# Optimization experiments

Measured on AMD Instinct MI355X. Metric: run time of the kernel, lower is better.

## Reference

```python
import jax, jax.numpy as jnp
import numpy as np


def _conv1x1(x_flat, W, b):
    # x_flat: [B, Cin, N], W: [Cout, Cin], b: [Cout]
    return jnp.einsum('oc,bcn->bon', W, x_flat) + b[None, :, None]


def setup_inputs() -> dict:
    key = jax.random.key(0)
    ks = jax.random.split(key, 7)
    B, C, H, W = 8, 64, 64, 64
    Ch = C // 2
    s_in = 1.0 / np.sqrt(C)
    x = jax.random.normal(ks[0], (B, C, H, W), dtype=jnp.float32)
    Wb = jax.random.uniform(ks[1], (Ch, C), jnp.float32, -s_in, s_in)
    bb = jax.random.uniform(ks[2], (Ch,), jnp.float32, -s_in, s_in)
    Wc = jax.random.uniform(ks[3], (Ch, C), jnp.float32, -s_in, s_in)
    bc = jax.random.uniform(ks[4], (Ch,), jnp.float32, -s_in, s_in)
    Wd = jax.random.uniform(ks[5], (C, C), jnp.float32, -s_in, s_in)
    bd = jax.random.uniform(ks[6], (C,), jnp.float32, -s_in, s_in)
    return {'x': x, 'Wb': Wb, 'bb': bb, 'Wc': Wc, 'bc': bc, 'Wd': Wd, 'bd': bd}


def reference(x, Wb, bb, Wc, bc, Wd, bd):
    B, C, H, Wd_ = x.shape
    N = H * Wd_
    x_flat = x.reshape(B, C, N)
    feat_b = _conv1x1(x_flat, Wb, bb)            # [B, C/2, N]
    feat_c = _conv1x1(x_flat, Wc, bc)            # [B, C/2, N]
    # scores[b,n,m] = sum_c feat_b[b,c,n] * feat_c[b,c,m]
    scores = jnp.einsum('bcn,bcm->bnm', feat_b, feat_c)
    attn = jax.nn.softmax(scores, axis=-1)       # [B, N, N]
    feat_d = _conv1x1(x_flat, Wd, bd)            # [B, C, N]
    # feat_e[b,c,m] = sum_n feat_d[b,c,n] * attn[b,m,n]  (bmm with attn^T)
    feat_e = jnp.einsum('bcn,bmn->bcm', feat_d, attn)
    return feat_e.reshape(B, C, H, Wd_) + x
```

## Files before the change

kernel.cpp:

```cpp
#include <hip/hip_runtime.h>

#define N_TOK 4096
#define L2E 1.44269504088896340736f

typedef short bf16x8 __attribute__((ext_vector_type(8)));
typedef float f32x4 __attribute__((ext_vector_type(4)));
typedef float f32x16 __attribute__((ext_vector_type(16)));
typedef unsigned int u32x4 __attribute__((ext_vector_type(4)));
typedef unsigned short u16x4 __attribute__((ext_vector_type(4)));

static __device__ __forceinline__ unsigned short f2bf(float f) {
    unsigned int u = __builtin_bit_cast(unsigned int, f);
    u += 0x7FFFu + ((u >> 16) & 1u);
    return (unsigned short)(u >> 16);
}

__global__ __launch_bounds__(256) void proj_kernel(
    const float* __restrict__ x,
    const float* __restrict__ Wb, const float* __restrict__ bb,
    const float* __restrict__ Wc, const float* __restrict__ bc,
    const float* __restrict__ Wd, const float* __restrict__ bd,
    unsigned short* __restrict__ Qg, unsigned short* __restrict__ Kg,
    unsigned short* __restrict__ VgT)
{
    const int b   = blockIdx.y;
    const int n0  = blockIdx.x * 64;
    const int tid = threadIdx.x;

    __shared__ unsigned short Wl[128 * 72];
    __shared__ unsigned short xT[64 * 72];
    __shared__ float bl[128];

    #pragma unroll
    for (int i = 0; i < 32; ++i) {
        int e = i * 256 + tid;
        int row = e >> 6, c = e & 63;
        float v;
        if (row < 32)      v = Wb[row * 64 + c];
        else if (row < 64) v = Wc[(row - 32) * 64 + c];
        else               v = Wd[(row - 64) * 64 + c];
        Wl[row * 72 + c] = f2bf(v);
    }
    if (tid < 128) {
        float v;
        if (tid < 32)      v = bb[tid];
        else if (tid < 64) v = bc[tid - 32];
        else               v = bd[tid - 64];
        bl[tid] = v;
    }
    #pragma unroll
    for (int i = 0; i < 16; ++i) {
        int e = i * 256 + tid;
        int c = e >> 6, nn = e & 63;
        xT[nn * 72 + c] = f2bf(x[((b * 64 + c) << 12) + n0 + nn]);
    }
    __syncthreads();

    const int w = tid >> 6, l = tid & 63;
    const int lrow = l & 15, lk = (l >> 4) * 8;

    const f32x4 vzero = {0.f, 0.f, 0.f, 0.f};
    f32x4 acc[2][4];
    #pragma unroll
    for (int rt = 0; rt < 2; ++rt)
        #pragma unroll
        for (int ct = 0; ct < 4; ++ct)
            acc[rt][ct] = vzero;

    #pragma unroll
    for (int kb = 0; kb < 2; ++kb) {
        bf16x8 af[2];
        #pragma unroll
        for (int rt = 0; rt < 2; ++rt)
            af[rt] = *(const bf16x8*)&Wl[(w * 32 + rt * 16 + lrow) * 72 + kb * 32 + lk];
        #pragma unroll
        for (int ct = 0; ct < 4; ++ct) {
            bf16x8 bfr = *(const bf16x8*)&xT[(ct * 16 + lrow) * 72 + kb * 32 + lk];
            #pragma unroll
            for (int rt = 0; rt < 2; ++rt)
                acc[rt][ct] = __builtin_amdgcn_mfma_f32_16x16x32_bf16(af[rt], bfr, acc[rt][ct], 0, 0, 0);
        }
    }

    #pragma unroll
    for (int rt = 0; rt < 2; ++rt) {
        const int row0 = w * 32 + rt * 16 + ((l >> 4) << 2);
        #pragma unroll
        for (int ct = 0; ct < 4; ++ct) {
            const int n = n0 + ct * 16 + lrow;
            if (row0 < 64) {
                u16x4 pk;
                #pragma unroll
                for (int r = 0; r < 4; ++r) {
                    float v = acc[rt][ct][r] + bl[row0 + r];
                    if (row0 < 32) v *= L2E;
                    pk[r] = f2bf(v);
                }
                unsigned short* dst = (row0 < 32)
                    ? Qg + (size_t)(b * N_TOK + n) * 32 + row0
                    : Kg + (size_t)(b * N_TOK + n) * 32 + (row0 - 32);
                *(u16x4*)dst = pk;
            } else {
                #pragma unroll
                for (int r = 0; r < 4; ++r)
                    VgT[((size_t)(b * 64 + row0 - 64 + r) << 12) + n] =
                        f2bf(acc[rt][ct][r] + bl[row0 + r]);
            }
        }
    }
}

template <int NHALF>
__global__ __launch_bounds__(256) void attn_kernel(
    const unsigned short* __restrict__ Qg,
    const unsigned short* __restrict__ Kg,
    const unsigned short* __restrict__ VgT,
    const float* __restrict__ x,
    float* __restrict__ outp,
    float* __restrict__ Opart,
    float* __restrict__ Ppart)
{
    const int nwg = 256 * NHALF;
    int i = blockIdx.x;
    int wg = (i & 7) * (nwg >> 3) + (i >> 3);
    const int b    = wg / (32 * NHALF);
    const int rem  = wg % (32 * NHALF);
    const int half = (NHALF >= 2) ? (rem >> 5) : 0;
    const int qblk = (NHALF >= 2) ? (rem & 31) : rem;
    const int q0   = qblk * 128;
    const int jbase = half * (N_TOK / NHALF);
    const int NT    = (N_TOK / NHALF) / 64;

    const int tid = threadIdx.x;
    const int w  = tid >> 6, l = tid & 63;
    const int lc = l & 31, hi = l >> 5;

    __shared__ unsigned short Kl[2][64 * 36];
    __shared__ unsigned short Vt[2][64 * 68];
    __shared__ float den[4][32];

    bf16x8 qf[2];
    #pragma unroll
    for (int kb = 0; kb < 2; ++kb)
        qf[kb] = *(const bf16x8*)&Qg[(size_t)(b * N_TOK + q0 + w * 32 + lc) * 32 + kb * 16 + hi * 8];

    const int kj = tid >> 2, kseg = (tid & 3) * 8;
    const int vc = tid >> 2, vj   = (tid & 3) * 16;
    const size_t kbase = (size_t)(b * N_TOK + jbase + kj) * 32 + kseg;
    const size_t vbase = ((size_t)(b * 64 + vc) << 12) + jbase + vj;

    u32x4 kreg, vreg0, vreg1;

    kreg  = *(const u32x4*)&Kg[kbase];
    vreg0 = *(const u32x4*)&VgT[vbase];
    vreg1 = *(const u32x4*)&VgT[vbase + 8];
    *(u32x4*)&Kl[0][kj * 36 + kseg]   = kreg;
    *(u32x4*)&Vt[0][vc * 68 + vj]     = vreg0;
    *(u32x4*)&Vt[0][vc * 68 + vj + 8] = vreg1;
    if (NT > 1) {
        kreg  = *(const u32x4*)&Kg[kbase + 64 * 32];
        vreg0 = *(const u32x4*)&VgT[vbase + 64];
        vreg1 = *(const u32x4*)&VgT[vbase + 64 + 8];
    }
    __syncthreads();

    const f32x16 z16 = {0.f,0.f,0.f,0.f,0.f,0.f,0.f,0.f,0.f,0.f,0.f,0.f,0.f,0.f,0.f,0.f};
    f32x16 o[2] = {z16, z16};
    float psum = 0.f;

    for (int t = 0; t < NT; ++t) {
        const int cur = t & 1;

        f32x16 s[2];
        __builtin_amdgcn_s_setprio(1);
        #pragma unroll
        for (int jt = 0; jt < 2; ++jt) {
            bf16x8 kf0 = *(const bf16x8*)&Kl[cur][(jt * 32 + lc) * 36 + hi * 8];
            bf16x8 kf1 = *(const bf16x8*)&Kl[cur][(jt * 32 + lc) * 36 + 16 + hi * 8];
            s[jt] = __builtin_amdgcn_mfma_f32_32x32x16_bf16(kf0, qf[0], z16, 0, 0, 0);
            s[jt] = __builtin_amdgcn_mfma_f32_32x32x16_bf16(kf1, qf[1], s[jt], 0, 0, 0);
        }
        __builtin_amdgcn_s_setprio(0);

        unsigned paw[4][4];
        #pragma unroll
        for (int jt = 0; jt < 2; ++jt) {
            float pp[16];
            #pragma unroll
            for (int r = 0; r < 16; ++r) {
                float pv = __builtin_amdgcn_exp2f(s[jt][r]);
                psum += pv;
                pp[r] = pv;
            }
            #pragma unroll
            for (int kb2 = 0; kb2 < 2; ++kb2) {
                const int e = kb2 * 8;
                unsigned A, B, C, D;
                asm("v_cvt_pk_bf16_f32 %0, %1, %2" : "=v"(A) : "v"(pp[e + 0]), "v"(pp[e + 1]));
                asm("v_cvt_pk_bf16_f32 %0, %1, %2" : "=v"(B) : "v"(pp[e + 2]), "v"(pp[e + 3]));
                asm("v_cvt_pk_bf16_f32 %0, %1, %2" : "=v"(C) : "v"(pp[e + 4]), "v"(pp[e + 5]));
                asm("v_cvt_pk_bf16_f32 %0, %1, %2" : "=v"(D) : "v"(pp[e + 6]), "v"(pp[e + 7]));
                asm("v_permlane32_swap_b32 %0, %1" : "+v"(A), "+v"(C));
                asm("v_permlane32_swap_b32 %0, %1" : "+v"(B), "+v"(D));
                paw[jt * 2 + kb2][0] = A; paw[jt * 2 + kb2][1] = B;
                paw[jt * 2 + kb2][2] = C; paw[jt * 2 + kb2][3] = D;
            }
        }

        if (t + 1 < NT) {
            const int alt = cur ^ 1;
            *(u32x4*)&Kl[alt][kj * 36 + kseg]   = kreg;
            *(u32x4*)&Vt[alt][vc * 68 + vj]     = vreg0;
            *(u32x4*)&Vt[alt][vc * 68 + vj + 8] = vreg1;
            if (t + 2 < NT) {
                const int j2 = (t + 2) * 64;
                kreg  = *(const u32x4*)&Kg[kbase + (size_t)j2 * 32];
                vreg0 = *(const u32x4*)&VgT[vbase + j2];
                vreg1 = *(const u32x4*)&VgT[vbase + j2 + 8];
            }
        }

        __builtin_amdgcn_s_setprio(1);
        #pragma unroll
        for (int kb = 0; kb < 4; ++kb) {
            u32x4 pw = {paw[kb][0], paw[kb][1], paw[kb][2], paw[kb][3]};
            bf16x8 pa = __builtin_bit_cast(bf16x8, pw);
            #pragma unroll
            for (int cb = 0; cb < 2; ++cb) {
                bf16x8 vf = *(const bf16x8*)&Vt[cur][(cb * 32 + lc) * 68 + kb * 16 + hi * 8];
                o[cb] = __builtin_amdgcn_mfma_f32_32x32x16_bf16(pa, vf, o[cb], 0, 0, 0);
            }
        }
        __builtin_amdgcn_s_setprio(0);
        __syncthreads();
    }

    float tot = psum + __shfl_xor(psum, 32, 64);

    if (NHALF == 1) {
        if (hi == 0) den[w][lc] = __builtin_amdgcn_rcpf(tot);
        __syncthreads();
        #pragma unroll
        for (int cb = 0; cb < 2; ++cb) {
            const int c = cb * 32 + lc;
            #pragma unroll
            for (int g2 = 0; g2 < 4; ++g2) {
                const int qb = q0 + w * 32 + g2 * 8 + hi * 4;
                f32x4 rinv = *(const f32x4*)&den[w][g2 * 8 + hi * 4];
                const size_t idx = (size_t)(b * 64 + c) * N_TOK + qb;
                f32x4 xv = *(const f32x4*)&x[idx];
                f32x4 ov;
                #pragma unroll
                for (int r = 0; r < 4; ++r)
                    ov[r] = o[cb][g2 * 4 + r] * rinv[r] + xv[r];
                *(f32x4*)&outp[idx] = ov;
            }
        }
    } else {
        #pragma unroll
        for (int cb = 0; cb < 2; ++cb) {
            const size_t cidx = (size_t)((half * 8 + b) * 64 + cb * 32 + lc) * N_TOK;
            #pragma unroll
            for (int g2 = 0; g2 < 4; ++g2) {
                const int qb = q0 + w * 32 + g2 * 8 + hi * 4;
                f32x4 ov = {o[cb][g2 * 4 + 0], o[cb][g2 * 4 + 1],
                            o[cb][g2 * 4 + 2], o[cb][g2 * 4 + 3]};
                *(f32x4*)&Opart[cidx + qb] = ov;
            }
        }
        if (hi == 0)
            Ppart[(size_t)(half * 8 + b) * N_TOK + q0 + w * 32 + lc] = tot;
    }
}

template <int NHALF>
__global__ __launch_bounds__(256) void combine_kernel(
    const float* __restrict__ Opart, const float* __restrict__ Ppart,
    const float* __restrict__ x, float* __restrict__ outp)
{
    const int i = blockIdx.x * 256 + threadIdx.x;
    const int q  = (i & 1023) << 2;
    const int bc = i >> 10;
    const int b  = bc >> 6;
    const size_t obase = ((size_t)bc << 12) + q;

    f32x4 osum = {0.f, 0.f, 0.f, 0.f};
    f32x4 psum = {0.f, 0.f, 0.f, 0.f};
    #pragma unroll
    for (int h = 0; h < NHALF; ++h) {
        f32x4 oh = *(const f32x4*)&Opart[((size_t)h << 21) + obase];
        f32x4 ph = *(const f32x4*)&Ppart[((size_t)(h * 8 + b) << 12) + q];
        #pragma unroll
        for (int r = 0; r < 4; ++r) { osum[r] += oh[r]; psum[r] += ph[r]; }
    }
    f32x4 xv = *(const f32x4*)&x[obase];
    f32x4 ov;
    #pragma unroll
    for (int r = 0; r < 4; ++r)
        ov[r] = osum[r] * __builtin_amdgcn_rcpf(psum[r]) + xv[r];
    *(f32x4*)&outp[obase] = ov;
}

extern "C" void kernel_launch(void* const* d_in, const int* in_sizes, int n_in,
                              void* d_out, int out_size, void* d_ws, size_t ws_size,
                              hipStream_t stream) {
    const float* x  = (const float*)d_in[0];
    const float* Wb = (const float*)d_in[1];
    const float* bb = (const float*)d_in[2];
    const float* Wc = (const float*)d_in[3];
    const float* bc = (const float*)d_in[4];
    const float* Wd = (const float*)d_in[5];
    const float* bd = (const float*)d_in[6];
    float* out = (float*)d_out;

    unsigned short* Qg  = (unsigned short*)d_ws;
    unsigned short* Kg  = Qg + (size_t)8 * N_TOK * 32;
    unsigned short* VgT = Kg + (size_t)8 * N_TOK * 32;
    float* Opart = (float*)((char*)d_ws + (size_t)8 * 1024 * 1024);

    proj_kernel<<<dim3(64, 8), 256, 0, stream>>>(x, Wb, bb, Wc, bc, Wd, bd, Qg, Kg, VgT);

    if (ws_size >= (size_t)41 * 1024 * 1024) {
        float* Ppart = (float*)((char*)d_ws + (size_t)40 * 1024 * 1024);
        attn_kernel<4><<<1024, 256, 0, stream>>>(Qg, Kg, VgT, x, out, Opart, Ppart);
        combine_kernel<4><<<2048, 256, 0, stream>>>(Opart, Ppart, x, out);
    } else if (ws_size >= (size_t)25 * 1024 * 1024) {
        float* Ppart = (float*)((char*)d_ws + (size_t)24 * 1024 * 1024);
        attn_kernel<2><<<512, 256, 0, stream>>>(Qg, Kg, VgT, x, out, Opart, Ppart);
        combine_kernel<2><<<2048, 256, 0, stream>>>(Opart, Ppart, x, out);
    } else {
        attn_kernel<1><<<256, 256, 0, stream>>>(Qg, Kg, VgT, x, out, nullptr, nullptr);
    }
}
```

Baseline: 62.12 us.

## Use single-wave attention blocks reading K/V directly, store bf16 partials

```diff
diff --git a/kernel.cpp b/kernel.cpp
--- a/kernel.cpp
+++ b/kernel.cpp
@@ -13,6 +13,9 @@
     unsigned int u = __builtin_bit_cast(unsigned int, f);
     u += 0x7FFFu + ((u >> 16) & 1u);
     return (unsigned short)(u >> 16);
+}
+static __device__ __forceinline__ float bf2f(unsigned short v) {
+    return __builtin_bit_cast(float, ((unsigned)v) << 16);
 }
 
 __global__ __launch_bounds__(256) void proj_kernel(
@@ -111,85 +114,68 @@
 }
 
 template <int NHALF>
-__global__ __launch_bounds__(256) void attn_kernel(
+__global__ __launch_bounds__(64, 4) void attn_kernel(
     const unsigned short* __restrict__ Qg,
     const unsigned short* __restrict__ Kg,
     const unsigned short* __restrict__ VgT,
     const float* __restrict__ x,
     float* __restrict__ outp,
-    float* __restrict__ Opart,
+    unsigned short* __restrict__ Opart,
     float* __restrict__ Ppart)
 {
-    const int nwg = 256 * NHALF;
-    int i = blockIdx.x;
-    int wg = (i & 7) * (nwg >> 3) + (i >> 3);
-    const int b    = wg / (32 * NHALF);
-    const int rem  = wg % (32 * NHALF);
-    const int half = (NHALF >= 2) ? (rem >> 5) : 0;
-    const int qblk = (NHALF >= 2) ? (rem & 31) : rem;
-    const int q0   = qblk * 128;
+    const int nwg = 1024 * NHALF;
+    const int i0 = blockIdx.x;
+    const int wg = (i0 & 7) * (nwg >> 3) + (i0 >> 3);
+    const int bpb  = 128 * NHALF;
+    const int b    = wg / bpb;
+    const int rem  = wg % bpb;
+    const int half = (NHALF == 1) ? 0 : (rem >> 7);
+    const int qblk = rem & 127;
+    const int q0   = qblk * 32;
     const int jbase = half * (N_TOK / NHALF);
     const int NT    = (N_TOK / NHALF) / 64;
 
     const int tid = threadIdx.x;
-    const int w  = tid >> 6, l = tid & 63;
-    const int lc = l & 31, hi = l >> 5;
-
-    __shared__ unsigned short Kl[2][64 * 36];
-    __shared__ unsigned short Vt[2][64 * 68];
-    __shared__ float den[4][32];
-
-    bf16x8 qf[2];
-    #pragma unroll
-    for (int kb = 0; kb < 2; ++kb)
-        qf[kb] = *(const bf16x8*)&Qg[(size_t)(b * N_TOK + q0 + w * 32 + lc) * 32 + kb * 16 + hi * 8];
-
-    const int kj = tid >> 2, kseg = (tid & 3) * 8;
-    const int vc = tid >> 2, vj   = (tid & 3) * 16;
-    const size_t kbase = (size_t)(b * N_TOK + jbase + kj) * 32 + kseg;
-    const size_t vbase = ((size_t)(b * 64 + vc) << 12) + jbase + vj;
-
-    u32x4 kreg, vreg0, vreg1;
-
-    kreg  = *(const u32x4*)&Kg[kbase];
-    vreg0 = *(const u32x4*)&VgT[vbase];
-    vreg1 = *(const u32x4*)&VgT[vbase + 8];
-    *(u32x4*)&Kl[0][kj * 36 + kseg]   = kreg;
-    *(u32x4*)&Vt[0][vc * 68 + vj]     = vreg0;
-    *(u32x4*)&Vt[0][vc * 68 + vj + 8] = vreg1;
-    if (NT > 1) {
-        kreg  = *(const u32x4*)&Kg[kbase + 64 * 32];
-        vreg0 = *(const u32x4*)&VgT[vbase + 64];
-        vreg1 = *(const u32x4*)&VgT[vbase + 64 + 8];
-    }
-    __syncthreads();
+    const int lc = tid & 31, hi = tid >> 5;
+
+    __shared__ float den[32];
+
+    const unsigned short* qp = Qg + (size_t)(b * N_TOK + q0 + lc) * 32 + hi * 8;
+    const bf16x8 qf0 = *(const bf16x8*)qp;
+    const bf16x8 qf1 = *(const bf16x8*)(qp + 16);
+
+    const unsigned short* Kb = Kg + (size_t)(b * N_TOK + jbase) * 32;
+    const unsigned short* Vb = VgT + ((size_t)(b * 64) << 12) + jbase;
 
     const f32x16 z16 = {0.f,0.f,0.f,0.f,0.f,0.f,0.f,0.f,0.f,0.f,0.f,0.f,0.f,0.f,0.f,0.f};
-    f32x16 o[2] = {z16, z16};
-    float psum = 0.f;
+    f32x16 o0 = z16, o1 = z16;
+    float ps0 = 0.f, ps1 = 0.f;
 
     for (int t = 0; t < NT; ++t) {
-        const int cur = t & 1;
-
-        f32x16 s[2];
+        const int j0 = t * 64;
+
+        const unsigned short* kp = Kb + (size_t)(j0 + lc) * 32 + hi * 8;
+        bf16x8 k00 = *(const bf16x8*)(kp);
+        bf16x8 k01 = *(const bf16x8*)(kp + 16);
+        bf16x8 k10 = *(const bf16x8*)(kp + 32 * 32);
+        bf16x8 k11 = *(const bf16x8*)(kp + 32 * 32 + 16);
+
         __builtin_amdgcn_s_setprio(1);
+        f32x16 s0 = __builtin_amdgcn_mfma_f32_32x32x16_bf16(k00, qf0, z16, 0, 0, 0);
+        s0 = __builtin_amdgcn_mfma_f32_32x32x16_bf16(k01, qf1, s0, 0, 0, 0);
+        f32x16 s1 = __builtin_amdgcn_mfma_f32_32x32x16_bf16(k10, qf0, z16, 0, 0, 0);
+        s1 = __builtin_amdgcn_mfma_f32_32x32x16_bf16(k11, qf1, s1, 0, 0, 0);
+        __builtin_amdgcn_s_setprio(0);
+
+        u32x4 pa[4];
         #pragma unroll
         for (int jt = 0; jt < 2; ++jt) {
-            bf16x8 kf0 = *(const bf16x8*)&Kl[cur][(jt * 32 + lc) * 36 + hi * 8];
-            bf16x8 kf1 = *(const bf16x8*)&Kl[cur][(jt * 32 + lc) * 36 + 16 + hi * 8];
-            s[jt] = __builtin_amdgcn_mfma_f32_32x32x16_bf16(kf0, qf[0], z16, 0, 0, 0);
-            s[jt] = __builtin_amdgcn_mfma_f32_32x32x16_bf16(kf1, qf[1], s[jt], 0, 0, 0);
-        }
-        __builtin_amdgcn_s_setprio(0);
-
-        unsigned paw[4][4];
-        #pragma unroll
-        for (int jt = 0; jt < 2; ++jt) {
+            const f32x16& sv = jt ? s1 : s0;
             float pp[16];
             #pragma unroll
             for (int r = 0; r < 16; ++r) {
-                float pv = __builtin_amdgcn_exp2f(s[jt][r]);
-                psum += pv;
+                float pv = __builtin_amdgcn_exp2f(sv[r]);
+                if (r & 1) ps1 += pv; else ps0 += pv;
                 pp[r] = pv;
             }
             #pragma unroll
@@ -202,80 +188,70 @@
                 asm("v_cvt_pk_bf16_f32 %0, %1, %2" : "=v"(D) : "v"(pp[e + 6]), "v"(pp[e + 7]));
                 asm("v_permlane32_swap_b32 %0, %1" : "+v"(A), "+v"(C));
                 asm("v_permlane32_swap_b32 %0, %1" : "+v"(B), "+v"(D));
-                paw[jt * 2 + kb2][0] = A; paw[jt * 2 + kb2][1] = B;
-                paw[jt * 2 + kb2][2] = C; paw[jt * 2 + kb2][3] = D;
-            }
-        }
-
-        if (t + 1 < NT) {
-            const int alt = cur ^ 1;
-            *(u32x4*)&Kl[alt][kj * 36 + kseg]   = kreg;
-            *(u32x4*)&Vt[alt][vc * 68 + vj]     = vreg0;
-            *(u32x4*)&Vt[alt][vc * 68 + vj + 8] = vreg1;
-            if (t + 2 < NT) {
-                const int j2 = (t + 2) * 64;
-                kreg  = *(const u32x4*)&Kg[kbase + (size_t)j2 * 32];
-                vreg0 = *(const u32x4*)&VgT[vbase + j2];
-                vreg1 = *(const u32x4*)&VgT[vbase + j2 + 8];
-            }
-        }
-
+                pa[jt * 2 + kb2][0] = A; pa[jt * 2 + kb2][1] = B;
+                pa[jt * 2 + kb2][2] = C; pa[jt * 2 + kb2][3] = D;
+            }
+        }
+
+        const unsigned short* vp = Vb + ((size_t)lc << 12) + j0 + hi * 8;
         __builtin_amdgcn_s_setprio(1);
         #pragma unroll
         for (int kb = 0; kb < 4; ++kb) {
-            u32x4 pw = {paw[kb][0], paw[kb][1], paw[kb][2], paw[kb][3]};
-            bf16x8 pa = __builtin_bit_cast(bf16x8, pw);
-            #pragma unroll
-            for (int cb = 0; cb < 2; ++cb) {
-                bf16x8 vf = *(const bf16x8*)&Vt[cur][(cb * 32 + lc) * 68 + kb * 16 + hi * 8];
-                o[cb] = __builtin_amdgcn_mfma_f32_32x32x16_bf16(pa, vf, o[cb], 0, 0, 0);
-            }
+            bf16x8 pf = __builtin_bit_cast(bf16x8, pa[kb]);
+            bf16x8 vf0 = *(const bf16x8*)(vp + kb * 16);
+            bf16x8 vf1 = *(const bf16x8*)(vp + ((size_t)32 << 12) + kb * 16);
+            o0 = __builtin_amdgcn_mfma_f32_32x32x16_bf16(pf, vf0, o0, 0, 0, 0);
+            o1 = __builtin_amdgcn_mfma_f32_32x32x16_bf16(pf, vf1, o1, 0, 0, 0);
         }
         __builtin_amdgcn_s_setprio(0);
+    }
+
+    float ps = ps0 + ps1;
+    float tot = ps + __shfl_xor(ps, 32, 64);
+
+    if (NHALF == 1) {
+        if (hi == 0) den[lc] = __builtin_amdgcn_rcpf(tot);
         __syncthreads();
-    }
-
-    float tot = psum + __shfl_xor(psum, 32, 64);
-
-    if (NHALF == 1) {
-        if (hi == 0) den[w][lc] = __builtin_amdgcn_rcpf(tot);
-        __syncthreads();
         #pragma unroll
         for (int cb = 0; cb < 2; ++cb) {
+            const f32x16& ov16 = cb ? o1 : o0;
             const int c = cb * 32 + lc;
             #pragma unroll
             for (int g2 = 0; g2 < 4; ++g2) {
-                const int qb = q0 + w * 32 + g2 * 8 + hi * 4;
-                f32x4 rinv = *(const f32x4*)&den[w][g2 * 8 + hi * 4];
+                const int qb = q0 + g2 * 8 + hi * 4;
+                f32x4 rinv = *(const f32x4*)&den[g2 * 8 + hi * 4];
                 const size_t idx = (size_t)(b * 64 + c) * N_TOK + qb;
                 f32x4 xv = *(const f32x4*)&x[idx];
                 f32x4 ov;
                 #pragma unroll
                 for (int r = 0; r < 4; ++r)
-                    ov[r] = o[cb][g2 * 4 + r] * rinv[r] + xv[r];
+                    ov[r] = ov16[g2 * 4 + r] * rinv[r] + xv[r];
                 *(f32x4*)&outp[idx] = ov;
             }
         }
     } else {
         #pragma unroll
         for (int cb = 0; cb < 2; ++cb) {
-            const size_t cidx = (size_t)((half * 8 + b) * 64 + cb * 32 + lc) * N_TOK;
+            const f32x16& ov16 = cb ? o1 : o0;
+            unsigned short* obase =
+                Opart + ((size_t)((half * 8 + b) * 64 + cb * 32 + lc) << 12);
             #pragma unroll
             for (int g2 = 0; g2 < 4; ++g2) {
-                const int qb = q0 + w * 32 + g2 * 8 + hi * 4;
-                f32x4 ov = {o[cb][g2 * 4 + 0], o[cb][g2 * 4 + 1],
-                            o[cb][g2 * 4 + 2], o[cb][g2 * 4 + 3]};
-                *(f32x4*)&Opart[cidx + qb] = ov;
+                const int qb = q0 + g2 * 8 + hi * 4;
+                u16x4 pk;
+                #pragma unroll
+                for (int r = 0; r < 4; ++r) pk[r] = f2bf(ov16[g2 * 4 + r]);
+                *(u16x4*)(obase + qb) = pk;
             }
         }
         if (hi == 0)
-            Ppart[(size_t)(half * 8 + b) * N_TOK + q0 + w * 32 + lc] = tot;
+            Ppart[((size_t)(half * 8 + b) << 12) + q0 + lc] = tot;
     }
 }
 
 template <int NHALF>
 __global__ __launch_bounds__(256) void combine_kernel(
-    const float* __restrict__ Opart, const float* __restrict__ Ppart,
+    const unsigned short* __restrict__ Opart, const float* __restrict__ Ppart,
     const float* __restrict__ x, float* __restrict__ outp)
 {
     const int i = blockIdx.x * 256 + threadIdx.x;
@@ -288,10 +264,10 @@
     f32x4 psum = {0.f, 0.f, 0.f, 0.f};
     #pragma unroll
     for (int h = 0; h < NHALF; ++h) {
-        f32x4 oh = *(const f32x4*)&Opart[((size_t)h << 21) + obase];
-        f32x4 ph = *(const f32x4*)&Ppart[((size_t)(h * 8 + b) << 12) + q];
-        #pragma unroll
-        for (int r = 0; r < 4; ++r) { osum[r] += oh[r]; psum[r] += ph[r]; }
+        u16x4 oh = *(const u16x4*)&Opart[(((size_t)(h * 512 + bc)) << 12) + q];
+        f32x4 ph = *(const f32x4*)&Ppart[(((size_t)(h * 8 + b)) << 12) + q];
+        #pragma unroll
+        for (int r = 0; r < 4; ++r) { osum[r] += bf2f(oh[r]); psum[r] += ph[r]; }
     }
     f32x4 xv = *(const f32x4*)&x[obase];
     f32x4 ov;
@@ -316,19 +292,15 @@
     unsigned short* Qg  = (unsigned short*)d_ws;
     unsigned short* Kg  = Qg + (size_t)8 * N_TOK * 32;
     unsigned short* VgT = Kg + (size_t)8 * N_TOK * 32;
-    float* Opart = (float*)((char*)d_ws + (size_t)8 * 1024 * 1024);
+    unsigned short* Opart = (unsigned short*)((char*)d_ws + (size_t)8 * 1024 * 1024);
+    float* Ppart = (float*)((char*)d_ws + (size_t)24 * 1024 * 1024);
 
     proj_kernel<<<dim3(64, 8), 256, 0, stream>>>(x, Wb, bb, Wc, bc, Wd, bd, Qg, Kg, VgT);
 
-    if (ws_size >= (size_t)41 * 1024 * 1024) {
-        float* Ppart = (float*)((char*)d_ws + (size_t)40 * 1024 * 1024);
-        attn_kernel<4><<<1024, 256, 0, stream>>>(Qg, Kg, VgT, x, out, Opart, Ppart);
+    if (ws_size >= (size_t)25 * 1024 * 1024) {
+        attn_kernel<4><<<4096, 64, 0, stream>>>(Qg, Kg, VgT, x, out, Opart, Ppart);
         combine_kernel<4><<<2048, 256, 0, stream>>>(Opart, Ppart, x, out);
-    } else if (ws_size >= (size_t)25 * 1024 * 1024) {
-        float* Ppart = (float*)((char*)d_ws + (size_t)24 * 1024 * 1024);
-        attn_kernel<2><<<512, 256, 0, stream>>>(Qg, Kg, VgT, x, out, Opart, Ppart);
-        combine_kernel<2><<<2048, 256, 0, stream>>>(Opart, Ppart, x, out);
     } else {
-        attn_kernel<1><<<256, 256, 0, stream>>>(Qg, Kg, VgT, x, out, nullptr, nullptr);
-    }
-}
+        attn_kernel<1><<<1024, 64, 0, stream>>>(Qg, Kg, VgT, x, out, nullptr, nullptr);
+    }
+}
```

Result: slower. 98.90 us (+59.2%).

## Software-pipeline QK MFMA across tiles, interleave exp with PV, store partials in bf16

Applied to the files above, without the earlier changes.

```diff
diff --git a/kernel.cpp b/kernel.cpp
--- a/kernel.cpp
+++ b/kernel.cpp
@@ -13,6 +13,9 @@
     unsigned int u = __builtin_bit_cast(unsigned int, f);
     u += 0x7FFFu + ((u >> 16) & 1u);
     return (unsigned short)(u >> 16);
+}
+static __device__ __forceinline__ float bf2f(unsigned short v) {
+    return __builtin_bit_cast(float, ((unsigned)v) << 16);
 }
 
 __global__ __launch_bounds__(256) void proj_kernel(
@@ -117,7 +120,7 @@
     const unsigned short* __restrict__ VgT,
     const float* __restrict__ x,
     float* __restrict__ outp,
-    float* __restrict__ Opart,
+    unsigned short* __restrict__ Opart,
     float* __restrict__ Ppart)
 {
     const int nwg = 256 * NHALF;
@@ -139,10 +142,9 @@
     __shared__ unsigned short Vt[2][64 * 68];
     __shared__ float den[4][32];
 
-    bf16x8 qf[2];
-    #pragma unroll
-    for (int kb = 0; kb < 2; ++kb)
-        qf[kb] = *(const bf16x8*)&Qg[(size_t)(b * N_TOK + q0 + w * 32 + lc) * 32 + kb * 16 + hi * 8];
+    const unsigned short* qp = Qg + (size_t)(b * N_TOK + q0 + w * 32 + lc) * 32 + hi * 8;
+    const bf16x8 qf0 = *(const bf16x8*)qp;
+    const bf16x8 qf1 = *(const bf16x8*)(qp + 16);
 
     const int kj = tid >> 2, kseg = (tid & 3) * 8;
     const int vc = tid >> 2, vj   = (tid & 3) * 16;
@@ -165,83 +167,91 @@
     __syncthreads();
 
     const f32x16 z16 = {0.f,0.f,0.f,0.f,0.f,0.f,0.f,0.f,0.f,0.f,0.f,0.f,0.f,0.f,0.f,0.f};
-    f32x16 o[2] = {z16, z16};
-    float psum = 0.f;
+    f32x16 o0 = z16, o1 = z16;
+    f32x16 s0, s1;
+    float ps0 = 0.f, ps1 = 0.f;
+
+    {
+        __builtin_amdgcn_s_setprio(1);
+        bf16x8 a00 = *(const bf16x8*)&Kl[0][(lc) * 36 + hi * 8];
+        bf16x8 a01 = *(const bf16x8*)&Kl[0][(lc) * 36 + 16 + hi * 8];
+        bf16x8 a10 = *(const bf16x8*)&Kl[0][(32 + lc) * 36 + hi * 8];
+        bf16x8 a11 = *(const bf16x8*)&Kl[0][(32 + lc) * 36 + 16 + hi * 8];
+        s0 = __builtin_amdgcn_mfma_f32_32x32x16_bf16(a00, qf0, z16, 0, 0, 0);
+        s0 = __builtin_amdgcn_mfma_f32_32x32x16_bf16(a01, qf1, s0, 0, 0, 0);
+        s1 = __builtin_amdgcn_mfma_f32_32x32x16_bf16(a10, qf0, z16, 0, 0, 0);
+        s1 = __builtin_amdgcn_mfma_f32_32x32x16_bf16(a11, qf1, s1, 0, 0, 0);
+        __builtin_amdgcn_s_setprio(0);
+    }
 
     for (int t = 0; t < NT; ++t) {
         const int cur = t & 1;
 
-        f32x16 s[2];
-        __builtin_amdgcn_s_setprio(1);
-        #pragma unroll
-        for (int jt = 0; jt < 2; ++jt) {
-            bf16x8 kf0 = *(const bf16x8*)&Kl[cur][(jt * 32 + lc) * 36 + hi * 8];
-            bf16x8 kf1 = *(const bf16x8*)&Kl[cur][(jt * 32 + lc) * 36 + 16 + hi * 8];
-            s[jt] = __builtin_amdgcn_mfma_f32_32x32x16_bf16(kf0, qf[0], z16, 0, 0, 0);
-            s[jt] = __builtin_amdgcn_mfma_f32_32x32x16_bf16(kf1, qf[1], s[jt], 0, 0, 0);
-        }
-        __builtin_amdgcn_s_setprio(0);
-
-        unsigned paw[4][4];
-        #pragma unroll
-        for (int jt = 0; jt < 2; ++jt) {
-            float pp[16];
+        if (t + 1 < NT) {
+            *(u32x4*)&Kl[cur ^ 1][kj * 36 + kseg]   = kreg;
+            *(u32x4*)&Vt[cur ^ 1][vc * 68 + vj]     = vreg0;
+            *(u32x4*)&Vt[cur ^ 1][vc * 68 + vj + 8] = vreg1;
+        }
+        if (t + 2 < NT) {
+            const int j2 = (t + 2) * 64;
+            kreg  = *(const u32x4*)&Kg[kbase + (size_t)j2 * 32];
+            vreg0 = *(const u32x4*)&VgT[vbase + j2];
+            vreg1 = *(const u32x4*)&VgT[vbase + j2 + 8];
+        }
+
+        #pragma unroll
+        for (int kb = 0; kb < 4; ++kb) {
+            const f32x16& sv = (kb >> 1) ? s1 : s0;
+            const int e = (kb & 1) * 8;
+            float p[8];
             #pragma unroll
-            for (int r = 0; r < 16; ++r) {
-                float pv = __builtin_amdgcn_exp2f(s[jt][r]);
-                psum += pv;
-                pp[r] = pv;
+            for (int r = 0; r < 8; ++r) {
+                p[r] = __builtin_amdgcn_exp2f(sv[e + r]);
+                if (r & 1) ps1 += p[r]; else ps0 += p[r];
             }
-            #pragma unroll
-            for (int kb2 = 0; kb2 < 2; ++kb2) {
-                const int e = kb2 * 8;
-                unsigned A, B, C, D;
-                asm("v_cvt_pk_bf16_f32 %0, %1, %2" : "=v"(A) : "v"(pp[e + 0]), "v"(pp[e + 1]));
-                asm("v_cvt_pk_bf16_f32 %0, %1, %2" : "=v"(B) : "v"(pp[e + 2]), "v"(pp[e + 3]));
-                asm("v_cvt_pk_bf16_f32 %0, %1, %2" : "=v"(C) : "v"(pp[e + 4]), "v"(pp[e + 5]));
-                asm("v_cvt_pk_bf16_f32 %0, %1, %2" : "=v"(D) : "v"(pp[e + 6]), "v"(pp[e + 7]));
-                asm("v_permlane32_swap_b32 %0, %1" : "+v"(A), "+v"(C));
-                asm("v_permlane32_swap_b32 %0, %1" : "+v"(B), "+v"(D));
-                paw[jt * 2 + kb2][0] = A; paw[jt * 2 + kb2][1] = B;
-                paw[jt * 2 + kb2][2] = C; paw[jt * 2 + kb2][3] = D;
-            }
-        }
+            unsigned A, B, C, D;
+            asm("v_cvt_pk_bf16_f32 %0, %1, %2" : "=v"(A) : "v"(p[0]), "v"(p[1]));
+            asm("v_cvt_pk_bf16_f32 %0, %1, %2" : "=v"(B) : "v"(p[2]), "v"(p[3]));
+            asm("v_cvt_pk_bf16_f32 %0, %1, %2" : "=v"(C) : "v"(p[4]), "v"(p[5]));
+            asm("v_cvt_pk_bf16_f32 %0, %1, %2" : "=v"(D) : "v"(p[6]), "v"(p[7]));
+            asm("v_permlane32_swap_b32 %0, %1" : "+v"(A), "+v"(C));
+            asm("v_permlane32_swap_b32 %0, %1" : "+v"(B), "+v"(D));
+            u32x4 pw = {A, B, C, D};
+            bf16x8 pf = __builtin_bit_cast(bf16x8, pw);
+            bf16x8 vf0 = *(const bf16x8*)&Vt[cur][(lc) * 68 + kb * 16 + hi * 8];
+            bf16x8 vf1 = *(const bf16x8*)&Vt[cur][(32 + lc) * 68 + kb * 16 + hi * 8];
+            __builtin_amdgcn_s_setprio(1);
+            o0 = __builtin_amdgcn_mfma_f32_32x32x16_bf16(pf, vf0, o0, 0, 0, 0);
+            o1 = __builtin_amdgcn_mfma_f32_32x32x16_bf16(pf, vf1, o1, 0, 0, 0);
+            __builtin_amdgcn_s_setprio(0);
+        }
+
+        __syncthreads();
 
         if (t + 1 < NT) {
-            const int alt = cur ^ 1;
-            *(u32x4*)&Kl[alt][kj * 36 + kseg]   = kreg;
-            *(u32x4*)&Vt[alt][vc * 68 + vj]     = vreg0;
-            *(u32x4*)&Vt[alt][vc * 68 + vj + 8] = vreg1;
-            if (t + 2 < NT) {
-                const int j2 = (t + 2) * 64;
-                kreg  = *(const u32x4*)&Kg[kbase + (size_t)j2 * 32];
-                vreg0 = *(const u32x4*)&VgT[vbase + j2];
-                vreg1 = *(const u32x4*)&VgT[vbase + j2 + 8];
-            }
-        }
-
-        __builtin_amdgcn_s_setprio(1);
-        #pragma unroll
-        for (int kb = 0; kb < 4; ++kb) {
-            u32x4 pw = {paw[kb][0], paw[kb][1], paw[kb][2], paw[kb][3]};
-            bf16x8 pa = __builtin_bit_cast(bf16x8, pw);
-            #pragma unroll
-            for (int cb = 0; cb < 2; ++cb) {
-                bf16x8 vf = *(const bf16x8*)&Vt[cur][(cb * 32 + lc) * 68 + kb * 16 + hi * 8];
-                o[cb] = __builtin_amdgcn_mfma_f32_32x32x16_bf16(pa, vf, o[cb], 0, 0, 0);
-            }
-        }
-        __builtin_amdgcn_s_setprio(0);
-        __syncthreads();
-    }
-
-    float tot = psum + __shfl_xor(psum, 32, 64);
+            const int nxt = cur ^ 1;
+            __builtin_amdgcn_s_setprio(1);
+            bf16x8 a00 = *(const bf16x8*)&Kl[nxt][(lc) * 36 + hi * 8];
+            bf16x8 a01 = *(const bf16x8*)&Kl[nxt][(lc) * 36 + 16 + hi * 8];
+            bf16x8 a10 = *(const bf16x8*)&Kl[nxt][(32 + lc) * 36 + hi * 8];
+            bf16x8 a11 = *(const bf16x8*)&Kl[nxt][(32 + lc) * 36 + 16 + hi * 8];
+            s0 = __builtin_amdgcn_mfma_f32_32x32x16_bf16(a00, qf0, z16, 0, 0, 0);
+            s0 = __builtin_amdgcn_mfma_f32_32x32x16_bf16(a01, qf1, s0, 0, 0, 0);
+            s1 = __builtin_amdgcn_mfma_f32_32x32x16_bf16(a10, qf0, z16, 0, 0, 0);
+            s1 = __builtin_amdgcn_mfma_f32_32x32x16_bf16(a11, qf1, s1, 0, 0, 0);
+            __builtin_amdgcn_s_setprio(0);
+        }
+    }
+
+    float ps = ps0 + ps1;
+    float tot = ps + __shfl_xor(ps, 32, 64);
 
     if (NHALF == 1) {
         if (hi == 0) den[w][lc] = __builtin_amdgcn_rcpf(tot);
         __syncthreads();
         #pragma unroll
         for (int cb = 0; cb < 2; ++cb) {
+            const f32x16& ov16 = cb ? o1 : o0;
             const int c = cb * 32 + lc;
             #pragma unroll
             for (int g2 = 0; g2 < 4; ++g2) {
@@ -252,30 +262,33 @@
                 f32x4 ov;
                 #pragma unroll
                 for (int r = 0; r < 4; ++r)
-                    ov[r] = o[cb][g2 * 4 + r] * rinv[r] + xv[r];
+                    ov[r] = ov16[g2 * 4 + r] * rinv[r] + xv[r];
                 *(f32x4*)&outp[idx] = ov;
             }
         }
     } else {
         #pragma unroll
         for (int cb = 0; cb < 2; ++cb) {
-            const size_t cidx = (size_t)((half * 8 + b) * 64 + cb * 32 + lc) * N_TOK;
+            const f32x16& ov16 = cb ? o1 : o0;
+            unsigned short* obase =
+                Opart + ((size_t)((half * 8 + b) * 64 + cb * 32 + lc) << 12);
             #pragma unroll
             for (int g2 = 0; g2 < 4; ++g2) {
                 const int qb = q0 + w * 32 + g2 * 8 + hi * 4;
-                f32x4 ov = {o[cb][g2 * 4 + 0], o[cb][g2 * 4 + 1],
-                            o[cb][g2 * 4 + 2], o[cb][g2 * 4 + 3]};
-                *(f32x4*)&Opart[cidx + qb] = ov;
+                u16x4 pk;
+                #pragma unroll
+                for (int r = 0; r < 4; ++r) pk[r] = f2bf(ov16[g2 * 4 + r]);
+                *(u16x4*)(obase + qb) = pk;
             }
         }
         if (hi == 0)
-            Ppart[(size_t)(half * 8 + b) * N_TOK + q0 + w * 32 + lc] = tot;
+            Ppart[((size_t)(half * 8 + b) << 12) + q0 + w * 32 + lc] = tot;
     }
 }
 
 template <int NHALF>
 __global__ __launch_bounds__(256) void combine_kernel(
-    const float* __restrict__ Opart, const float* __restrict__ Ppart,
+    const unsigned short* __restrict__ Opart, const float* __restrict__ Ppart,
     const float* __restrict__ x, float* __restrict__ outp)
 {
     const int i = blockIdx.x * 256 + threadIdx.x;
@@ -288,10 +301,10 @@
     f32x4 psum = {0.f, 0.f, 0.f, 0.f};
     #pragma unroll
     for (int h = 0; h < NHALF; ++h) {
-        f32x4 oh = *(const f32x4*)&Opart[((size_t)h << 21) + obase];
-        f32x4 ph = *(const f32x4*)&Ppart[((size_t)(h * 8 + b) << 12) + q];
-        #pragma unroll
-        for (int r = 0; r < 4; ++r) { osum[r] += oh[r]; psum[r] += ph[r]; }
+        u16x4 oh = *(const u16x4*)&Opart[(((size_t)(h * 512 + bc)) << 12) + q];
+        f32x4 ph = *(const f32x4*)&Ppart[(((size_t)(h * 8 + b)) << 12) + q];
+        #pragma unroll
+        for (int r = 0; r < 4; ++r) { osum[r] += bf2f(oh[r]); psum[r] += ph[r]; }
     }
     f32x4 xv = *(const f32x4*)&x[obase];
     f32x4 ov;
@@ -316,18 +329,14 @@
     unsigned short* Qg  = (unsigned short*)d_ws;
     unsigned short* Kg  = Qg + (size_t)8 * N_TOK * 32;
     unsigned short* VgT = Kg + (size_t)8 * N_TOK * 32;
-    float* Opart = (float*)((char*)d_ws + (size_t)8 * 1024 * 1024);
+    unsigned short* Opart = (unsigned short*)((char*)d_ws + (size_t)8 * 1024 * 1024);
+    float* Ppart = (float*)((char*)d_ws + (size_t)24 * 1024 * 1024);
 
     proj_kernel<<<dim3(64, 8), 256, 0, stream>>>(x, Wb, bb, Wc, bc, Wd, bd, Qg, Kg, VgT);
 
-    if (ws_size >= (size_t)41 * 1024 * 1024) {
-        float* Ppart = (float*)((char*)d_ws + (size_t)40 * 1024 * 1024);
+    if (ws_size >= (size_t)25 * 1024 * 1024) {
         attn_kernel<4><<<1024, 256, 0, stream>>>(Qg, Kg, VgT, x, out, Opart, Ppart);
         combine_kernel<4><<<2048, 256, 0, stream>>>(Opart, Ppart, x, out);
-    } else if (ws_size >= (size_t)25 * 1024 * 1024) {
-        float* Ppart = (float*)((char*)d_ws + (size_t)24 * 1024 * 1024);
-        attn_kernel<2><<<512, 256, 0, stream>>>(Qg, Kg, VgT, x, out, Opart, Ppart);
-        combine_kernel<2><<<2048, 256, 0, stream>>>(Opart, Ppart, x, out);
     } else {
         attn_kernel<1><<<256, 256, 0, stream>>>(Qg, Kg, VgT, x, out, nullptr, nullptr);
     }
```

New measurement: 58.56 us. 1.06x faster.
